# Kernel optimization log

Measured on AMD Instinct MI355X. Metric: run time of the kernel, lower is better.

Reference implementation:

```python
import jax, jax.numpy as jnp
import numpy as np

H = 256          # h_dim
SEQ_LEN = 10     # max history length
B = 2048         # number of queries with non-empty history
N = 327680       # total flattened neighbors across all (query, timestep) segments
NUM_SEG = B * SEQ_LEN
NUM_ENT = 20000
NUM_REL = 200


def setup_inputs() -> dict:
    key = jax.random.key(0)
    ks = jax.random.split(key, 9)
    s = jax.random.randint(ks[0], (B,), 0, NUM_ENT)
    r = jax.random.randint(ks[1], (B,), 0, NUM_REL)
    nbr_ids = jax.random.randint(ks[2], (N,), 0, NUM_ENT)
    seg_ids = jnp.sort(jax.random.randint(ks[3], (N,), 0, NUM_SEG))
    ent_embeds = jax.random.normal(ks[4], (NUM_ENT, H), dtype=jnp.float32)
    rel_embeds = jax.random.normal(ks[5], (NUM_REL, H), dtype=jnp.float32)
    W_attn = jax.random.normal(ks[6], (3 * H, H), dtype=jnp.float32) * 0.05
    b_attn = jax.random.normal(ks[7], (H,), dtype=jnp.float32) * 0.05
    v_s = jax.random.normal(ks[8], (H, 1), dtype=jnp.float32) * 0.05
    return {"s": s, "r": r, "nbr_ids": nbr_ids, "seg_ids": seg_ids,
            "ent_embeds": ent_embeds, "rel_embeds": rel_embeds,
            "W_attn": W_attn, "b_attn": b_attn, "v_s": v_s}


def reference(s, r, nbr_ids, seg_ids, ent_embeds, rel_embeds, W_attn, b_attn, v_s):
    # Per-neighbor gathers. Each neighbor belongs to segment seg = q*SEQ_LEN + t.
    q = seg_ids // SEQ_LEN                              # query index per neighbor [N]
    em = ent_embeds[nbr_ids]                            # [N, H] neighbor embeddings
    s_emb = ent_embeds[s]                               # [B, H]
    r_emb = rel_embeds[r]                               # [B, H]
    ss = s_emb[q]                                       # [N, H]
    rr = r_emb[q]                                       # [N, H]
    # Score: tanh(Linear(3H -> H)) @ v_s  -> scalar per neighbor
    x = jnp.concatenate([em, ss, rr], axis=1)           # [N, 3H]
    scores = (jnp.tanh(x @ W_attn + b_attn) @ v_s)[:, 0]  # [N]
    # Segment softmax over neighbors within each (query, timestep) segment.
    m = jax.ops.segment_max(scores, seg_ids, num_segments=NUM_SEG)  # [S]
    e = jnp.exp(scores - m[seg_ids])                    # [N]
    denom = jax.ops.segment_sum(e, seg_ids, num_segments=NUM_SEG)   # [S]
    w = e / denom[seg_ids]                              # [N]
    # Weighted sum of neighbor embeddings per segment (scatter-reduce).
    agg = jax.ops.segment_sum(w[:, None] * em, seg_ids, num_segments=NUM_SEG)  # [S, H]
    counts = jax.ops.segment_sum(jnp.ones_like(scores), seg_ids, num_segments=NUM_SEG)
    mask = (counts > 0).astype(em.dtype).reshape(B, SEQ_LEN, 1)     # present timesteps
    agg = agg.reshape(B, SEQ_LEN, H)
    ss_t = jnp.broadcast_to(s_emb[:, None, :], (B, SEQ_LEN, H))
    rr_t = jnp.broadcast_to(r_emb[:, None, :], (B, SEQ_LEN, H))
    # Padded [B, SEQ_LEN, 3H] sequence tensor (rows for empty segments are zero,
    # matching the torch code's zero-initialized padded tensor). Dropout p=0.0.
    out = jnp.concatenate([agg, ss_t, rr_t], axis=2) * mask
    return out
```

## Files before the change

kernel.cpp:

```cpp
#include <hip/hip_runtime.h>
#include <hip/hip_bf16.h>

#define H 256
#define SEQ 10
#define C2LOG2E 2.8853900817779268f
#define LOG2E 1.4426950408889634f

typedef __attribute__((ext_vector_type(8))) short bf16x8;
typedef __attribute__((ext_vector_type(4))) float f32x4;

__device__ __forceinline__ unsigned short f2bf(float x) {
    union { float f; unsigned u; } v; v.f = x;
    unsigned r = v.u + 0x7fff + ((v.u >> 16) & 1);
    return (unsigned short)(r >> 16);
}
__device__ __forceinline__ float bf2f(unsigned short b) {
    union { unsigned u; float f; } v; v.u = ((unsigned)b) << 16;
    return v.f;
}
__device__ __forceinline__ float fexp2(float x) {
    return __builtin_amdgcn_exp2f(x);
}

__global__ void prep_kernel(const float* __restrict__ W,
                            unsigned short* __restrict__ Wt,
                            const int* __restrict__ seg_ids,
                            int* __restrict__ seg_start,
                            int nWt, int n, int num_seg) {
    if ((int)blockIdx.x < nWt) {
        int idx = blockIdx.x * 256 + threadIdx.x;
        if (idx >= H * 3 * H) return;
        int nn = idx / (3 * H), k = idx % (3 * H);
        Wt[idx] = f2bf(C2LOG2E * W[k * H + nn]);
    } else {
        int j = (blockIdx.x - nWt) * 256 + threadIdx.x;
        if (j >= n) return;
        int cur = seg_ids[j];
        int prev = (j == 0) ? -1 : seg_ids[j - 1];
        for (int s2 = prev + 1; s2 <= cur; s2++) seg_start[s2] = j;
        if (j == n - 1)
            for (int s2 = cur + 1; s2 <= num_seg; s2++) seg_start[s2] = n;
    }
}

__global__ void gemm_bf16_kernel(const float* __restrict__ entf,
                                 const int* __restrict__ sidx,
                                 const int* __restrict__ ridx,
                                 const float* __restrict__ rel,
                                 const unsigned short* __restrict__ Wt,
                                 const float* __restrict__ bias,
                                 unsigned short* __restrict__ comb,
                                 unsigned short* __restrict__ qpart,
                                 int nEntBlk, int M0, int M1) {
    __shared__ unsigned short As[64][40];
    bool isEnt = (int)blockIdx.x < nEntBlk;
    int m0 = (isEnt ? blockIdx.x : (blockIdx.x - nEntBlk)) * 64;
    int M = isEnt ? M0 : M1;
    int K = isEnt ? H : 2 * H;
    int k0 = isEnt ? 0 : H;
    int ldo = isEnt ? 512 : H;
    unsigned short* outp = isEnt ? comb : qpart;

    int t = threadIdx.x;
    int sr = t >> 2;
    int sc = (t & 3) * 8;
    int wave = t >> 6, lane = t & 63;
    int lr = lane & 15, lg = lane >> 4;

    f32x4 acc[4][4];
#pragma unroll
    for (int i = 0; i < 4; i++)
#pragma unroll
        for (int jn = 0; jn < 4; jn++) acc[i][jn] = (f32x4){0.f, 0.f, 0.f, 0.f};

    const unsigned short* bp[4];
#pragma unroll
    for (int bn = 0; bn < 4; bn++)
        bp[bn] = Wt + (size_t)(wave * 64 + bn * 16 + lr) * (3 * H) + k0 + lg * 8;

    for (int kk = 0; kk < K; kk += 32) {
        bf16x8 av = {};
        int gm = m0 + sr;
        if (gm < M) {
            const float* src;
            if (isEnt) {
                src = entf + (size_t)gm * H + kk + sc;
            } else {
                int k = kk + sc;
                src = (k < H) ? (entf + (size_t)sidx[gm] * H + k)
                              : (rel + (size_t)ridx[gm] * H + (k - H));
            }
            float4 f0 = *reinterpret_cast<const float4*>(src);
            float4 f1 = *reinterpret_cast<const float4*>(src + 4);
            av[0] = (short)f2bf(f0.x); av[1] = (short)f2bf(f0.y);
            av[2] = (short)f2bf(f0.z); av[3] = (short)f2bf(f0.w);
            av[4] = (short)f2bf(f1.x); av[5] = (short)f2bf(f1.y);
            av[6] = (short)f2bf(f1.z); av[7] = (short)f2bf(f1.w);
            if (isEnt)
                *reinterpret_cast<bf16x8*>(comb + (size_t)gm * 512 + 256 + kk + sc) = av;
        }
        *reinterpret_cast<bf16x8*>(&As[sr][sc]) = av;

        bf16x8 bfr[4];
#pragma unroll
        for (int bn = 0; bn < 4; bn++)
            bfr[bn] = *reinterpret_cast<const bf16x8*>(bp[bn] + kk);

        __syncthreads();
        bf16x8 afr[4];
#pragma unroll
        for (int am = 0; am < 4; am++)
            afr[am] = *reinterpret_cast<const bf16x8*>(&As[am * 16 + lr][lg * 8]);
#pragma unroll
        for (int am = 0; am < 4; am++)
#pragma unroll
            for (int bn = 0; bn < 4; bn++)
                acc[am][bn] = __builtin_amdgcn_mfma_f32_16x16x32_bf16(
                    afr[am], bfr[bn], acc[am][bn], 0, 0, 0);
        __syncthreads();
    }

#pragma unroll
    for (int bn = 0; bn < 4; bn++) {
        int col = wave * 64 + bn * 16 + lr;
        float bv = isEnt ? 0.f : C2LOG2E * bias[col];
#pragma unroll
        for (int am = 0; am < 4; am++) {
#pragma unroll
            for (int rr = 0; rr < 4; rr++) {
                int row = m0 + am * 16 + lg * 4 + rr;
                if (row < M)
                    outp[(size_t)row * ldo + col] = f2bf(acc[am][bn][rr] + bv);
            }
        }
    }
}

__global__ void __launch_bounds__(128)
fused_agg_kernel(const int* __restrict__ nbr_ids,
                 const int* __restrict__ seg_start,
                 const unsigned short* __restrict__ comb,
                 const unsigned short* __restrict__ qpartbf,
                 const float* __restrict__ v_s,
                 const float* __restrict__ ent_embeds,
                 const float* __restrict__ rel_embeds,
                 const int* __restrict__ s,
                 const int* __restrict__ r,
                 float* __restrict__ out, int num_seg) {
    int seg = blockIdx.x * 2 + (threadIdx.x >> 6);
    if (seg >= num_seg) return;
    int lane = threadIdx.x & 63;
    int g = lane >> 4, li = lane & 15;
    int cb = li * 16;
    int c4 = lane * 4;
    int b = seg / SEQ;
    int start = seg_start[seg], end = seg_start[seg + 1];
    float* orow = out + (size_t)seg * (3 * H);

    if (start == end) {
        float4 z = {0.f, 0.f, 0.f, 0.f};
        *reinterpret_cast<float4*>(orow + c4) = z;
        *reinterpret_cast<float4*>(orow + H + c4) = z;
        *reinterpret_cast<float4*>(orow + 2 * H + c4) = z;
        return;
    }

    float4 ssv = *reinterpret_cast<const float4*>(ent_embeds + (size_t)s[b] * H + c4);
    float4 rrv = *reinterpret_cast<const float4*>(rel_embeds + (size_t)r[b] * H + c4);

    float vm2[16];
    float vsum = 0.f;
    {
        const float4* vp = reinterpret_cast<const float4*>(v_s + cb);
#pragma unroll
        for (int k = 0; k < 4; k++) {
            float4 tv = vp[k];
            vm2[4 * k + 0] = -2.f * tv.x; vm2[4 * k + 1] = -2.f * tv.y;
            vm2[4 * k + 2] = -2.f * tv.z; vm2[4 * k + 3] = -2.f * tv.w;
            vsum += tv.x + tv.y + tv.z + tv.w;
        }
    }

    float qv[16];
    {
        bf16x8 qa = *reinterpret_cast<const bf16x8*>(qpartbf + (size_t)b * H + cb);
        bf16x8 qb = *reinterpret_cast<const bf16x8*>(qpartbf + (size_t)b * H + cb + 8);
#pragma unroll
        for (int k = 0; k < 8; k++) {
            qv[k] = bf2f((unsigned short)qa[k]);
            qv[8 + k] = bf2f((unsigned short)qb[k]);
        }
    }

    float acc[16];
#pragma unroll
    for (int k = 0; k < 16; k++) acc[k] = 0.f;
    float lpart = 0.f;

    int cc = end - start;
    int nitm = (cc + 3) >> 2;

    bf16x8 p0 = {}, p1 = {}, e0 = {}, e1 = {};
    if (g < cc) {
        const unsigned short* row = comb + (size_t)nbr_ids[start + g] * 512 + cb;
        p0 = *reinterpret_cast<const bf16x8*>(row);
        p1 = *reinterpret_cast<const bf16x8*>(row + 8);
        e0 = *reinterpret_cast<const bf16x8*>(row + 256);
        e1 = *reinterpret_cast<const bf16x8*>(row + 264);
    }

    for (int ji = 0; ji < nitm; ji++) {
        bf16x8 p0n = {}, p1n = {}, e0n = {}, e1n = {};
        int jn = 4 * (ji + 1) + g;
        if (jn < cc) {
            const unsigned short* rown = comb + (size_t)nbr_ids[start + jn] * 512 + cb;
            p0n = *reinterpret_cast<const bf16x8*>(rown);
            p1n = *reinterpret_cast<const bf16x8*>(rown + 8);
            e0n = *reinterpret_cast<const bf16x8*>(rown + 256);
            e1n = *reinterpret_cast<const bf16x8*>(rown + 264);
        }

        float sa = 0.f, sb = 0.f;
#pragma unroll
        for (int k = 0; k < 8; k += 2) {
            float a0 = fexp2(bf2f((unsigned short)p0[k]) + qv[k]) + 1.f;
            float a1 = fexp2(bf2f((unsigned short)p1[k]) + qv[8 + k]) + 1.f;
            float num = vm2[k] * a1;
            num = fmaf(vm2[8 + k], a0, num);
            sa = fmaf(num, __builtin_amdgcn_rcpf(a0 * a1), sa);
            float b0 = fexp2(bf2f((unsigned short)p0[k + 1]) + qv[k + 1]) + 1.f;
            float b1 = fexp2(bf2f((unsigned short)p1[k + 1]) + qv[9 + k]) + 1.f;
            float numb = vm2[k + 1] * b1;
            numb = fmaf(vm2[9 + k], b0, numb);
            sb = fmaf(numb, __builtin_amdgcn_rcpf(b0 * b1), sb);
        }
        float s16 = sa + sb + vsum;
        s16 += __shfl_xor(s16, 1);
        s16 += __shfl_xor(s16, 2);
        s16 += __shfl_xor(s16, 4);
        s16 += __shfl_xor(s16, 8);
        float e = fexp2(s16 * LOG2E);
        e = (4 * ji + g < cc) ? e : 0.f;
        lpart += e;
#pragma unroll
        for (int k = 0; k < 8; k++) {
            acc[k] = fmaf(e, bf2f((unsigned short)e0[k]), acc[k]);
            acc[8 + k] = fmaf(e, bf2f((unsigned short)e1[k]), acc[8 + k]);
        }
        p0 = p0n; p1 = p1n; e0 = e0n; e1 = e1n;
    }

    lpart += __shfl_xor(lpart, 16);
    lpart += __shfl_xor(lpart, 32);
#pragma unroll
    for (int k = 0; k < 16; k++) {
        acc[k] += __shfl_xor(acc[k], 16);
        acc[k] += __shfl_xor(acc[k], 32);
    }
    float invl = 1.f / lpart;

    float4 o;
#pragma unroll
    for (int k = 0; k < 4; k++) {
        float v0 = acc[k], v1 = acc[4 + k], v2 = acc[8 + k], v3 = acc[12 + k];
        float pick = (g == 0) ? v0 : (g == 1) ? v1 : (g == 2) ? v2 : v3;
        if (k == 0) o.x = pick * invl;
        else if (k == 1) o.y = pick * invl;
        else if (k == 2) o.z = pick * invl;
        else o.w = pick * invl;
    }
    *reinterpret_cast<float4*>(orow + cb + 4 * g) = o;
    *reinterpret_cast<float4*>(orow + H + c4) = ssv;
    *reinterpret_cast<float4*>(orow + 2 * H + c4) = rrv;
}

extern "C" void kernel_launch(void* const* d_in, const int* in_sizes, int n_in,
                              void* d_out, int out_size, void* d_ws, size_t ws_size,
                              hipStream_t stream) {
    const int* s = (const int*)d_in[0];
    const int* r = (const int*)d_in[1];
    const int* nbr_ids = (const int*)d_in[2];
    const int* seg_ids = (const int*)d_in[3];
    const float* ent_embeds = (const float*)d_in[4];
    const float* rel_embeds = (const float*)d_in[5];
    const float* W_attn = (const float*)d_in[6];
    const float* b_attn = (const float*)d_in[7];
    const float* v_s = (const float*)d_in[8];
    float* out = (float*)d_out;

    int B = in_sizes[0];
    int N = in_sizes[2];
    int num_ent = in_sizes[4] / H;
    int num_seg = B * SEQ;

    char* ws = (char*)d_ws;
    unsigned short* comb = (unsigned short*)ws;
    unsigned short* Wt = comb + (size_t)num_ent * 512;
    unsigned short* qpartbf = Wt + (size_t)H * 3 * H;
    int* seg_start = (int*)(qpartbf + (size_t)B * H);

    int nWt = (H * 3 * H + 255) / 256;
    int nSeg = (N + 255) / 256;
    prep_kernel<<<nWt + nSeg, 256, 0, stream>>>(W_attn, Wt, seg_ids, seg_start,
                                                nWt, N, num_seg);

    int nEntBlk = (num_ent + 63) / 64;
    int nQBlk = B / 64;
    gemm_bf16_kernel<<<nEntBlk + nQBlk, 256, 0, stream>>>(
        ent_embeds, s, r, rel_embeds, Wt, b_attn, comb, qpartbf,
        nEntBlk, num_ent, B);

    fused_agg_kernel<<<(num_seg + 1) / 2, 128, 0, stream>>>(
        nbr_ids, seg_start, comb, qpartbf, v_s,
        ent_embeds, rel_embeds, s, r, out, num_seg);
}
```

Baseline: 91.22 us.

## Tile W transpose via LDS, prefetch neighbor ids, use reduce-scatter shuffles

The W transpose in the prep kernel now stages 64x64 tiles through shared memory, so global reads and the bf16 writes are coalesced and vectorized instead of strided scalar accesses. The aggregation loop loads neighbor ids one iteration ahead, which takes the index load off the critical path of the dependent row gather. The final cross-lane accumulator reduction becomes a reduce-scatter that exchanges half the values per stage, roughly halving the shuffle count. The cost is extra shared-memory use and added index arithmetic.

```diff
diff --git a/kernel.cpp b/kernel.cpp
--- a/kernel.cpp
+++ b/kernel.cpp
@@ -26,14 +26,39 @@
                             unsigned short* __restrict__ Wt,
                             const int* __restrict__ seg_ids,
                             int* __restrict__ seg_start,
-                            int nWt, int n, int num_seg) {
-    if ((int)blockIdx.x < nWt) {
-        int idx = blockIdx.x * 256 + threadIdx.x;
-        if (idx >= H * 3 * H) return;
-        int nn = idx / (3 * H), k = idx % (3 * H);
-        Wt[idx] = f2bf(C2LOG2E * W[k * H + nn]);
+                            int nTr, int n, int num_seg) {
+    if ((int)blockIdx.x < nTr) {
+        __shared__ float tile[64][65];
+        int tk = blockIdx.x % 12;
+        int tn = blockIdx.x / 12;
+        int t = threadIdx.x;
+        int rr = t >> 2;
+        int rc = (t & 3) * 16;
+        const float* src = W + (size_t)(tk * 64 + rr) * H + tn * 64 + rc;
+        float4 a = *reinterpret_cast<const float4*>(src);
+        float4 b = *reinterpret_cast<const float4*>(src + 4);
+        float4 c = *reinterpret_cast<const float4*>(src + 8);
+        float4 d = *reinterpret_cast<const float4*>(src + 12);
+        tile[rr][rc + 0] = a.x;  tile[rr][rc + 1] = a.y;
+        tile[rr][rc + 2] = a.z;  tile[rr][rc + 3] = a.w;
+        tile[rr][rc + 4] = b.x;  tile[rr][rc + 5] = b.y;
+        tile[rr][rc + 6] = b.z;  tile[rr][rc + 7] = b.w;
+        tile[rr][rc + 8] = c.x;  tile[rr][rc + 9] = c.y;
+        tile[rr][rc + 10] = c.z; tile[rr][rc + 11] = c.w;
+        tile[rr][rc + 12] = d.x; tile[rr][rc + 13] = d.y;
+        tile[rr][rc + 14] = d.z; tile[rr][rc + 15] = d.w;
+        __syncthreads();
+        bf16x8 o0, o1;
+#pragma unroll
+        for (int j = 0; j < 8; j++) {
+            o0[j] = (short)f2bf(C2LOG2E * tile[rc + j][rr]);
+            o1[j] = (short)f2bf(C2LOG2E * tile[rc + 8 + j][rr]);
+        }
+        unsigned short* dst = Wt + (size_t)(tn * 64 + rr) * (3 * H) + tk * 64 + rc;
+        *reinterpret_cast<bf16x8*>(dst) = o0;
+        *reinterpret_cast<bf16x8*>(dst + 8) = o1;
     } else {
-        int j = (blockIdx.x - nWt) * 256 + threadIdx.x;
+        int j = (blockIdx.x - nTr) * 256 + threadIdx.x;
         if (j >= n) return;
         int cur = seg_ids[j];
         int prev = (j == 0) ? -1 : seg_ids[j - 1];
@@ -200,9 +225,12 @@
     int cc = end - start;
     int nitm = (cc + 3) >> 2;
 
+    int nbA = nbr_ids[start + min(g, cc - 1)];
+    int nbB = nbr_ids[start + min(4 + g, cc - 1)];
+
     bf16x8 p0 = {}, p1 = {}, e0 = {}, e1 = {};
     if (g < cc) {
-        const unsigned short* row = comb + (size_t)nbr_ids[start + g] * 512 + cb;
+        const unsigned short* row = comb + (size_t)nbA * 512 + cb;
         p0 = *reinterpret_cast<const bf16x8*>(row);
         p1 = *reinterpret_cast<const bf16x8*>(row + 8);
         e0 = *reinterpret_cast<const bf16x8*>(row + 256);
@@ -213,12 +241,13 @@
         bf16x8 p0n = {}, p1n = {}, e0n = {}, e1n = {};
         int jn = 4 * (ji + 1) + g;
         if (jn < cc) {
-            const unsigned short* rown = comb + (size_t)nbr_ids[start + jn] * 512 + cb;
+            const unsigned short* rown = comb + (size_t)nbB * 512 + cb;
             p0n = *reinterpret_cast<const bf16x8*>(rown);
             p1n = *reinterpret_cast<const bf16x8*>(rown + 8);
             e0n = *reinterpret_cast<const bf16x8*>(rown + 256);
             e1n = *reinterpret_cast<const bf16x8*>(rown + 264);
         }
+        int nbC = nbr_ids[start + min(4 * (ji + 2) + g, cc - 1)];
 
         float sa = 0.f, sb = 0.f;
 #pragma unroll
@@ -248,26 +277,33 @@
             acc[8 + k] = fmaf(e, bf2f((unsigned short)e1[k]), acc[8 + k]);
         }
         p0 = p0n; p1 = p1n; e0 = e0n; e1 = e1n;
+        nbB = nbC;
     }
 
     lpart += __shfl_xor(lpart, 16);
     lpart += __shfl_xor(lpart, 32);
-#pragma unroll
-    for (int k = 0; k < 16; k++) {
-        acc[k] += __shfl_xor(acc[k], 16);
-        acc[k] += __shfl_xor(acc[k], 32);
-    }
     float invl = 1.f / lpart;
 
+    int gb0 = g & 1, gb1 = g >> 1;
+    float t1[8];
+#pragma unroll
+    for (int j = 0; j < 8; j++) {
+        int sl0 = (j < 4) ? j : 4 + j;
+        int sl1 = sl0 + 4;
+        float mine = gb0 ? acc[sl1] : acc[sl0];
+        float opp  = gb0 ? acc[sl0] : acc[sl1];
+        t1[j] = mine + __shfl_xor(opp, 16);
+    }
     float4 o;
 #pragma unroll
-    for (int k = 0; k < 4; k++) {
-        float v0 = acc[k], v1 = acc[4 + k], v2 = acc[8 + k], v3 = acc[12 + k];
-        float pick = (g == 0) ? v0 : (g == 1) ? v1 : (g == 2) ? v2 : v3;
-        if (k == 0) o.x = pick * invl;
-        else if (k == 1) o.y = pick * invl;
-        else if (k == 2) o.z = pick * invl;
-        else o.w = pick * invl;
+    for (int j = 0; j < 4; j++) {
+        float mine = gb1 ? t1[4 + j] : t1[j];
+        float opp  = gb1 ? t1[j] : t1[4 + j];
+        float fin = (mine + __shfl_xor(opp, 32)) * invl;
+        if (j == 0) o.x = fin;
+        else if (j == 1) o.y = fin;
+        else if (j == 2) o.z = fin;
+        else o.w = fin;
     }
     *reinterpret_cast<float4*>(orow + cb + 4 * g) = o;
     *reinterpret_cast<float4*>(orow + H + c4) = ssv;
@@ -299,10 +335,10 @@
     unsigned short* qpartbf = Wt + (size_t)H * 3 * H;
     int* seg_start = (int*)(qpartbf + (size_t)B * H);
 
-    int nWt = (H * 3 * H + 255) / 256;
+    int nTr = 12 * 4;
     int nSeg = (N + 255) / 256;
-    prep_kernel<<<nWt + nSeg, 256, 0, stream>>>(W_attn, Wt, seg_ids, seg_start,
-                                                nWt, N, num_seg);
+    prep_kernel<<<nTr + nSeg, 256, 0, stream>>>(W_attn, Wt, seg_ids, seg_start,
+                                                nTr, N, num_seg);
 
     int nEntBlk = (num_ent + 63) / 64;
     int nQBlk = B / 64;
```

After: 98.10 us. 1.08x slower.
